# Optimization experiments

Measured on AMD Instinct MI355X. Metric: run time of the kernel, lower is better.

The kernel has to match this reference:

```python
import jax, jax.numpy as jnp
import numpy as np

B, N, FH, H, FO = 8, 1024, 128, 8, 64
FIN = 2 * FH  # f_hid * 2
NEG = -1e9
SLOPE = 0.2  # leaky_relu negative slope (GAT default)


def setup_inputs() -> dict:
    key = jax.random.key(0)
    ks = jax.random.split(key, 10)
    x = jax.random.normal(ks[0], (B, FIN), jnp.float32)
    A = jax.random.randint(ks[1], (B, N, N), 0, 2, jnp.int32)  # 0/1 dense adjacency
    mask_zero = jnp.ones((B, N, 1), jnp.float32)  # node validity mask
    p_atten = jax.random.uniform(ks[2], (B, N), jnp.float32)  # unused in forward body
    e_atten = jax.random.uniform(ks[3], (B, N, FIN), jnp.float32)
    Npost = jax.random.normal(ks[4], (N, FIN), jnp.float32) * np.float32(1.0 / np.sqrt(FIN))  # kaiming-ish
    w = jax.random.normal(ks[5], (H, FIN, FO), jnp.float32) * np.float32(1.0 / np.sqrt(FIN))
    a_src = jax.random.normal(ks[6], (H, FO), jnp.float32) * np.float32(0.1)
    a_dst = jax.random.normal(ks[7], (H, FO), jnp.float32) * np.float32(0.1)
    bias = jnp.zeros((FO,), jnp.float32)
    return {"x": x, "A": A, "mask_zero": mask_zero, "p_atten": p_atten,
            "e_atten": e_atten, "Npost": Npost, "w": w, "a_src": a_src,
            "a_dst": a_dst, "bias": bias}


def reference(x, A, mask_zero, p_atten, e_atten, Npost, w, a_src, a_dst, bias):
    # broadcast-mul feature gating: x [B,FIN] repeated over N posts, gated by Npost*e_atten
    recx = x[:, None, :] * (Npost[None, :, :] * e_atten)          # [B,N,FIN]
    # BatchGAT (DeepInf-style multi-head graph attention, dropout disabled / eval mode)
    h = jnp.einsum('bnf,hfo->bhno', recx, w)                      # [B,H,N,FO]
    s = jnp.einsum('bhno,ho->bhn', h, a_src)                      # src attention term
    d = jnp.einsum('bhno,ho->bhn', h, a_dst)                      # dst attention term
    logits = jax.nn.leaky_relu(s[:, :, :, None] + d[:, :, None, :], SLOPE)  # [B,H,N,N]
    adj = (A > 0)[:, None, :, :]                                  # [B,1,N,N]
    logits = jnp.where(adj, logits, NEG)
    attn = jax.nn.softmax(logits, axis=-1)                        # masked row softmax
    out = jnp.einsum('bhnm,bhmo->bhno', attn, h) + bias           # aggregate neighbors
    out = out.mean(axis=1)                                        # average heads -> [B,N,FO]
    return out * mask_zero                                        # zero padded nodes
```

## Files before the change

kernel.cpp:

```cpp
#include <hip/hip_runtime.h>

typedef __attribute__((ext_vector_type(8))) short          bf16x8;
typedef __attribute__((ext_vector_type(8))) unsigned short u16x8;
typedef __attribute__((ext_vector_type(4))) unsigned short u16x4;
typedef __attribute__((ext_vector_type(4))) float          f32x4;
typedef __attribute__((ext_vector_type(4))) unsigned int   u32x4;

union U8 { u16x8 u; bf16x8 b; u32x4 w; };
union U4 { u16x4 u; unsigned w[2]; };

__device__ __forceinline__ unsigned short f2bf(float f){
  unsigned u = __float_as_uint(f);
  return (unsigned short)((u + 0x7fffu + ((u >> 16) & 1u)) >> 16);
}
__device__ __forceinline__ unsigned pack_bf16(float lo, float hi){
  unsigned a = __float_as_uint(hi) + 0x8000u;
  unsigned b = __float_as_uint(lo) + 0x8000u;
  return __builtin_amdgcn_perm(a, b, 0x07060302u);
}
__device__ __forceinline__ unsigned maskpack(float e0, float e1, unsigned m){
  unsigned r;
  asm("v_cvt_pk_bf16_f32 %0, %1, %2" : "=v"(r) : "v"(e0), "v"(e1));
  return r & m;
}

#define NN  1024
#define FIN 256
#define NH  8
#define FO  64

__global__ __launch_bounds__(256) void stage0(
    const float* __restrict__ w, const int* __restrict__ A,
    unsigned short* __restrict__ wfrag, unsigned long long* __restrict__ Abits)
{
  const int tid = blockIdx.x * 256 + threadIdx.x;
  if (tid < 16384){
    const int lane = tid & 63, ss = (tid >> 6) & 3, kc = (tid >> 8) & 7, h = tid >> 11;
    const int o = 16 * ss + (lane & 15);
    const int f = kc * 32 + (lane >> 4) * 8;
    u16x8 r;
    #pragma unroll
    for (int j = 0; j < 8; j++) r[j] = f2bf(w[(h * FIN + f + j) * FO + o]);
    *(u16x8*)(wfrag + tid * 8) = r;
  }
  for (int i = tid; i < 8388608; i += 262144){
    unsigned long long m = __ballot(A[i] > 0);
    if ((threadIdx.x & 63) == 0) Abits[i >> 6] = m;
  }
}

__global__ __launch_bounds__(512, 4) void stageA(
    const float* __restrict__ x, const float* __restrict__ e_at,
    const float* __restrict__ Np, const unsigned short* __restrict__ wfrag,
    const float* __restrict__ a_src, const float* __restrict__ a_dst,
    unsigned short* __restrict__ hT,
    float* __restrict__ Rt, float* __restrict__ expd, float* __restrict__ expd2)
{
  __shared__ unsigned short rex[16 * 264];
  const int t = threadIdx.x;
  const int n0 = blockIdx.x * 16, b = blockIdx.y;

  {
    const int row = t >> 5, f0 = (t & 31) * 8;
    const int nrow = n0 + row;
    const float* ep = e_at + (b * NN + nrow) * FIN + f0;
    const float* qp = Np + nrow * FIN + f0;
    const float* xp = x + b * FIN + f0;
    f32x4 e0 = *(const f32x4*)ep, e1 = *(const f32x4*)(ep + 4);
    f32x4 q0 = *(const f32x4*)qp, q1 = *(const f32x4*)(qp + 4);
    f32x4 x0 = *(const f32x4*)xp, x1 = *(const f32x4*)(xp + 4);
    u16x8 r;
    #pragma unroll
    for (int j = 0; j < 4; j++){
      r[j]     = f2bf(e0[j] * q0[j] * x0[j]);
      r[j + 4] = f2bf(e1[j] * q1[j] * x1[j]);
    }
    *(u16x8*)(rex + row * 264 + f0) = r;
  }
  __syncthreads();

  const int h = t >> 6, lane = t & 63, quad = lane >> 4, l15 = lane & 15;
  const unsigned short* wf = wfrag + h * 16384 + lane * 8;

  f32x4 acc[4] = {};
  #pragma unroll
  for (int kc = 0; kc < 8; kc++){
    U8 a0, bf[4];
    a0.u = *(const u16x8*)(rex + l15 * 264 + kc * 32 + quad * 8);
    #pragma unroll
    for (int ss = 0; ss < 4; ss++) bf[ss].u = *(const u16x8*)(wf + (kc * 4 + ss) * 512);
    #pragma unroll
    for (int ss = 0; ss < 4; ss++)
      acc[ss] = __builtin_amdgcn_mfma_f32_16x16x32_bf16(a0.b, bf[ss].b, acc[ss], 0, 0, 0);
  }

  {
    const int mtile = blockIdx.x >> 1, moff = (blockIdx.x & 1) * 16;
    unsigned short* pan = hT + (size_t)(((b * NH + h) * 32 + mtile) * 64) * 32;
    #pragma unroll
    for (int ss = 0; ss < 4; ss++){
      U4 v;
      v.w[0] = pack_bf16(acc[ss][0], acc[ss][1]);
      v.w[1] = pack_bf16(acc[ss][2], acc[ss][3]);
      *(u16x4*)(pan + (16 * ss + l15) * 32 + moff + quad * 4) = v.u;
    }
  }

  float as4[4], ad4[4];
  #pragma unroll
  for (int ss = 0; ss < 4; ss++){
    as4[ss] = a_src[h * FO + 16 * ss + l15];
    ad4[ss] = a_dst[h * FO + 16 * ss + l15];
  }
  #pragma unroll
  for (int i = 0; i < 4; i++){
    float ps = 0.f, pd = 0.f;
    #pragma unroll
    for (int ss = 0; ss < 4; ss++){ ps += acc[ss][i] * as4[ss]; pd += acc[ss][i] * ad4[ss]; }
    #pragma unroll
    for (int off = 1; off < 16; off <<= 1){
      ps += __shfl_xor(ps, off);
      pd += __shfl_xor(pd, off);
    }
    if (l15 == 0){
      const int idx = (b * NH + h) * NN + n0 + quad * 4 + i;
      Rt[idx]    = __expf(0.8f * ps);
      expd[idx]  = __expf(pd);
      expd2[idx] = __expf(0.2f * pd);
    }
  }
}

__global__ __launch_bounds__(256, 4) void stageB(
    const unsigned* __restrict__ Aw,
    const unsigned short* __restrict__ hT,
    const float* __restrict__ Rt,
    const float* __restrict__ expd, const float* __restrict__ expd2,
    float* __restrict__ hpart)
{
  __shared__ float smem[4288];
  __shared__ __align__(8) unsigned lut[16][2];

  const int fid = blockIdx.x;
  const int b = fid & 7, h = (fid >> 3) & 7, rt = fid >> 6;
  const int n0 = rt * 64;

  const int t = threadIdx.x;
  const int w = t >> 6, lane = t & 63, quad = lane >> 4, l15 = lane & 15;
  const int rw = w & 1, mh = w >> 1;
  const int nb = n0 + rw * 32;

  if (t < 16){
    lut[t][0] = (t & 1 ? 0xFFFFu : 0u) | (t & 2 ? 0xFFFF0000u : 0u);
    lut[t][1] = (t & 4 ? 0xFFFFu : 0u) | (t & 8 ? 0xFFFF0000u : 0u);
  }
  {
    const float* s1 = expd  + (b * NH + h) * NN;
    const float* s2 = expd2 + (b * NH + h) * NN;
    *(f32x4*)(smem + t * 4)        = *(const f32x4*)(s1 + t * 4);
    *(f32x4*)(smem + 1024 + t * 4) = *(const f32x4*)(s2 + t * 4);
  }
  __syncthreads();

  const int hb = (b * NH + h) * NN;
  const float Rv0 = Rt[hb + nb + l15];
  const float Rv1 = Rt[hb + nb + 16 + l15];
  const unsigned short* pb = hT + (size_t)(b * NH + h) * 65536 + l15 * 32 + quad * 8;
  const float* edh = smem + quad * 8;
  const float* e2h = smem + 1024 + quad * 8;
  const unsigned* awp = Aw + (b * NN + nb) * 32;
  const int c0 = mh * 16;
  const int qs = quad * 8;

  U8 pan[4];
  #pragma unroll
  for (int ss = 0; ss < 4; ss++)
    pan[ss].u = *(const u16x8*)(pb + (size_t)c0 * 2048 + ss * 512);
  unsigned mw0 = awp[l15 * 32 + c0];
  unsigned mw1 = awp[(16 + l15) * 32 + c0];

  U8 ones;
  #pragma unroll
  for (int j = 0; j < 8; j++) ones.u[j] = 0x3F80;

  f32x4 acc0[4] = {}, acc1[4] = {};
  f32x4 accl0 = {}, accl1 = {};

  for (int cc = 0; cc < 16; cc++){
    const int c = c0 + cc;
    const unsigned am0 = (mw0 >> qs) & 0xFF;
    const unsigned am1 = (mw1 >> qs) & 0xFF;
    const uint2 la0 = *(const uint2*)&lut[am0 & 15][0];
    const uint2 lb0 = *(const uint2*)&lut[(am0 >> 4) & 15][0];
    const uint2 la1 = *(const uint2*)&lut[am1 & 15][0];
    const uint2 lb1 = *(const uint2*)&lut[(am1 >> 4) & 15][0];
    if (cc + 1 < 16){
      mw0 = awp[l15 * 32 + c + 1];
      mw1 = awp[(16 + l15) * 32 + c + 1];
    }
    const f32x4 d01 = *(const f32x4*)(edh + c * 32);
    const f32x4 d23 = *(const f32x4*)(edh + c * 32 + 4);
    const f32x4 g01 = *(const f32x4*)(e2h + c * 32);
    const f32x4 g23 = *(const f32x4*)(e2h + c * 32 + 4);
    {
      const f32x4 p01 = Rv0 * d01, p23 = Rv0 * d23;
      U8 p;
      p.w[0] = maskpack(fmaxf(p01[0], g01[0]), fmaxf(p01[1], g01[1]), la0.x);
      p.w[1] = maskpack(fmaxf(p01[2], g01[2]), fmaxf(p01[3], g01[3]), la0.y);
      p.w[2] = maskpack(fmaxf(p23[0], g23[0]), fmaxf(p23[1], g23[1]), lb0.x);
      p.w[3] = maskpack(fmaxf(p23[2], g23[2]), fmaxf(p23[3], g23[3]), lb0.y);
      #pragma unroll
      for (int ss = 0; ss < 4; ss++)
        acc0[ss] = __builtin_amdgcn_mfma_f32_16x16x32_bf16(p.b, pan[ss].b, acc0[ss], 0, 0, 0);
      accl0 = __builtin_amdgcn_mfma_f32_16x16x32_bf16(p.b, ones.b, accl0, 0, 0, 0);
    }
    {
      const f32x4 p01 = Rv1 * d01, p23 = Rv1 * d23;
      U8 p;
      p.w[0] = maskpack(fmaxf(p01[0], g01[0]), fmaxf(p01[1], g01[1]), la1.x);
      p.w[1] = maskpack(fmaxf(p01[2], g01[2]), fmaxf(p01[3], g01[3]), la1.y);
      p.w[2] = maskpack(fmaxf(p23[0], g23[0]), fmaxf(p23[1], g23[1]), lb1.x);
      p.w[3] = maskpack(fmaxf(p23[2], g23[2]), fmaxf(p23[3], g23[3]), lb1.y);
      #pragma unroll
      for (int ss = 0; ss < 4; ss++)
        acc1[ss] = __builtin_amdgcn_mfma_f32_16x16x32_bf16(p.b, pan[ss].b, acc1[ss], 0, 0, 0);
      accl1 = __builtin_amdgcn_mfma_f32_16x16x32_bf16(p.b, ones.b, accl1, 0, 0, 0);
    }
    if (cc + 1 < 16){
      #pragma unroll
      for (int ss = 0; ss < 4; ss++)
        pan[ss].u = *(const u16x8*)(pb + (size_t)(c + 1) * 2048 + ss * 512);
    }
  }

  __syncthreads();

  float* den = smem + 4160;
  if (l15 == 0){
    #pragma unroll
    for (int i = 0; i < 4; i++){
      den[mh * 64 + rw * 32 + quad * 4 + i]      = accl0[i];
      den[mh * 64 + rw * 32 + 16 + quad * 4 + i] = accl1[i];
    }
  }
  if (mh == 1){
    #pragma unroll
    for (int i = 0; i < 4; i++){
      const int r0 = rw * 32 + quad * 4 + i;
      #pragma unroll
      for (int ss = 0; ss < 4; ss++){
        smem[r0 * 65 + ss * 16 + l15]        = acc0[ss][i];
        smem[(r0 + 16) * 65 + ss * 16 + l15] = acc1[ss][i];
      }
    }
  }
  __syncthreads();

  if (mh == 0){
    float* hp = hpart + ((size_t)(b * NH + h) * NN + nb) * FO;
    #pragma unroll
    for (int i = 0; i < 4; i++){
      const int r = quad * 4 + i;
      const float ia = 1.0f / (den[rw * 32 + r] + den[64 + rw * 32 + r]);
      const float ib = 1.0f / (den[rw * 32 + 16 + r] + den[64 + rw * 32 + 16 + r]);
      #pragma unroll
      for (int ss = 0; ss < 4; ss++){
        hp[(size_t)r * FO + ss * 16 + l15] =
            (acc0[ss][i] + smem[(rw * 32 + r) * 65 + ss * 16 + l15]) * ia;
        hp[(size_t)(16 + r) * FO + ss * 16 + l15] =
            (acc1[ss][i] + smem[(rw * 32 + 16 + r) * 65 + ss * 16 + l15]) * ib;
      }
    }
  }
}

__global__ __launch_bounds__(256) void stageC(
    const float* __restrict__ hpart, const float* __restrict__ bias,
    const float* __restrict__ mz, float* __restrict__ out)
{
  const int tid = blockIdx.x * 256 + threadIdx.x;
  const int o4 = (tid & 15) * 4;
  const int n  = (tid >> 4) & 1023;
  const int b  = tid >> 14;
  const size_t nf = (size_t)n * FO + o4;
  f32x4 s = {};
  #pragma unroll
  for (int h = 0; h < NH; h++)
    s += *(const f32x4*)(hpart + (size_t)(b * NH + h) * NN * FO + nf);
  const f32x4 bv = *(const f32x4*)(bias + o4);
  const float m = mz[b * NN + n];
  f32x4 r;
  #pragma unroll
  for (int j = 0; j < 4; j++) r[j] = (0.125f * s[j] + bv[j]) * m;
  *(f32x4*)(out + (size_t)b * NN * FO + nf) = r;
}

extern "C" void kernel_launch(void* const* d_in, const int* in_sizes, int n_in,
                              void* d_out, int out_size, void* d_ws, size_t ws_size,
                              hipStream_t stream)
{
  (void)in_sizes; (void)n_in; (void)out_size; (void)ws_size;
  const float* x    = (const float*)d_in[0];
  const int*   A    = (const int*)d_in[1];
  const float* mz   = (const float*)d_in[2];
  const float* e_at = (const float*)d_in[4];
  const float* Np   = (const float*)d_in[5];
  const float* w    = (const float*)d_in[6];
  const float* asrc = (const float*)d_in[7];
  const float* adst = (const float*)d_in[8];
  const float* bias = (const float*)d_in[9];
  float* out = (float*)d_out;

  char* ws = (char*)d_ws;
  unsigned short* wfrag = (unsigned short*)ws;
  unsigned short* hT    = (unsigned short*)(ws + 262144);
  float* Rt    = (float*)(ws + 8650752);
  float* expd  = (float*)(ws + 8912896);
  float* expd2 = (float*)(ws + 9175040);
  unsigned long long* Abits = (unsigned long long*)(ws + 9437184);
  float* hpart = (float*)(ws + 10485760);

  stage0<<<dim3(1024), dim3(256), 0, stream>>>(w, A, wfrag, Abits);
  stageA<<<dim3(64, 8), dim3(512), 0, stream>>>(x, e_at, Np, wfrag, asrc, adst,
                                                hT, Rt, expd, expd2);
  stageB<<<dim3(1024), dim3(256), 0, stream>>>((const unsigned*)Abits, hT,
                                               Rt, expd, expd2, hpart);
  stageC<<<dim3(512), dim3(256), 0, stream>>>(hpart, bias, mz, out);
}
```

Baseline: 153.0 us.

## Move adjacency bit-packing into stageA and double-buffer stageB panel loads

```diff
diff --git a/kernel.cpp b/kernel.cpp
--- a/kernel.cpp
+++ b/kernel.cpp
@@ -30,29 +30,23 @@
 #define FO  64
 
 __global__ __launch_bounds__(256) void stage0(
-    const float* __restrict__ w, const int* __restrict__ A,
-    unsigned short* __restrict__ wfrag, unsigned long long* __restrict__ Abits)
+    const float* __restrict__ w, unsigned short* __restrict__ wfrag)
 {
   const int tid = blockIdx.x * 256 + threadIdx.x;
-  if (tid < 16384){
-    const int lane = tid & 63, ss = (tid >> 6) & 3, kc = (tid >> 8) & 7, h = tid >> 11;
-    const int o = 16 * ss + (lane & 15);
-    const int f = kc * 32 + (lane >> 4) * 8;
-    u16x8 r;
-    #pragma unroll
-    for (int j = 0; j < 8; j++) r[j] = f2bf(w[(h * FIN + f + j) * FO + o]);
-    *(u16x8*)(wfrag + tid * 8) = r;
-  }
-  for (int i = tid; i < 8388608; i += 262144){
-    unsigned long long m = __ballot(A[i] > 0);
-    if ((threadIdx.x & 63) == 0) Abits[i >> 6] = m;
-  }
+  const int lane = tid & 63, ss = (tid >> 6) & 3, kc = (tid >> 8) & 7, h = tid >> 11;
+  const int o = 16 * ss + (lane & 15);
+  const int f = kc * 32 + (lane >> 4) * 8;
+  u16x8 r;
+  #pragma unroll
+  for (int j = 0; j < 8; j++) r[j] = f2bf(w[(h * FIN + f + j) * FO + o]);
+  *(u16x8*)(wfrag + tid * 8) = r;
 }
 
 __global__ __launch_bounds__(512, 4) void stageA(
     const float* __restrict__ x, const float* __restrict__ e_at,
     const float* __restrict__ Np, const unsigned short* __restrict__ wfrag,
     const float* __restrict__ a_src, const float* __restrict__ a_dst,
+    const int* __restrict__ A, unsigned long long* __restrict__ Abits,
     unsigned short* __restrict__ hT,
     float* __restrict__ Rt, float* __restrict__ expd, float* __restrict__ expd2)
 {
@@ -129,6 +123,16 @@
       expd2[idx] = __expf(0.2f * pd);
     }
   }
+
+  {
+    const int seg = (b * 64 + blockIdx.x) * 16384;
+    #pragma unroll 4
+    for (int k = 0; k < 32; k++){
+      const int i = seg + k * 512 + t;
+      unsigned long long m = __ballot(A[i] > 0);
+      if ((t & 63) == 0) Abits[i >> 6] = m;
+    }
+  }
 }
 
 __global__ __launch_bounds__(256, 4) void stageB(
@@ -172,12 +176,13 @@
   const int c0 = mh * 16;
   const int qs = quad * 8;
 
-  U8 pan[4];
+  U8 panc[4], pann[4];
   #pragma unroll
   for (int ss = 0; ss < 4; ss++)
-    pan[ss].u = *(const u16x8*)(pb + (size_t)c0 * 2048 + ss * 512);
-  unsigned mw0 = awp[l15 * 32 + c0];
-  unsigned mw1 = awp[(16 + l15) * 32 + c0];
+    panc[ss].u = *(const u16x8*)(pb + (size_t)c0 * 2048 + ss * 512);
+  unsigned mwc0 = awp[l15 * 32 + c0];
+  unsigned mwc1 = awp[(16 + l15) * 32 + c0];
+  unsigned mwn0, mwn1;
 
   U8 ones;
   #pragma unroll
@@ -186,18 +191,22 @@
   f32x4 acc0[4] = {}, acc1[4] = {};
   f32x4 accl0 = {}, accl1 = {};
 
+  #pragma unroll
   for (int cc = 0; cc < 16; cc++){
     const int c = c0 + cc;
-    const unsigned am0 = (mw0 >> qs) & 0xFF;
-    const unsigned am1 = (mw1 >> qs) & 0xFF;
+    if (cc + 1 < 16){
+      #pragma unroll
+      for (int ss = 0; ss < 4; ss++)
+        pann[ss].u = *(const u16x8*)(pb + (size_t)(c + 1) * 2048 + ss * 512);
+      mwn0 = awp[l15 * 32 + c + 1];
+      mwn1 = awp[(16 + l15) * 32 + c + 1];
+    }
+    const unsigned am0 = (mwc0 >> qs) & 0xFF;
+    const unsigned am1 = (mwc1 >> qs) & 0xFF;
     const uint2 la0 = *(const uint2*)&lut[am0 & 15][0];
     const uint2 lb0 = *(const uint2*)&lut[(am0 >> 4) & 15][0];
     const uint2 la1 = *(const uint2*)&lut[am1 & 15][0];
     const uint2 lb1 = *(const uint2*)&lut[(am1 >> 4) & 15][0];
-    if (cc + 1 < 16){
-      mw0 = awp[l15 * 32 + c + 1];
-      mw1 = awp[(16 + l15) * 32 + c + 1];
-    }
     const f32x4 d01 = *(const f32x4*)(edh + c * 32);
     const f32x4 d23 = *(const f32x4*)(edh + c * 32 + 4);
     const f32x4 g01 = *(const f32x4*)(e2h + c * 32);
@@ -211,7 +220,7 @@
       p.w[3] = maskpack(fmaxf(p23[2], g23[2]), fmaxf(p23[3], g23[3]), lb0.y);
       #pragma unroll
       for (int ss = 0; ss < 4; ss++)
-        acc0[ss] = __builtin_amdgcn_mfma_f32_16x16x32_bf16(p.b, pan[ss].b, acc0[ss], 0, 0, 0);
+        acc0[ss] = __builtin_amdgcn_mfma_f32_16x16x32_bf16(p.b, panc[ss].b, acc0[ss], 0, 0, 0);
       accl0 = __builtin_amdgcn_mfma_f32_16x16x32_bf16(p.b, ones.b, accl0, 0, 0, 0);
     }
     {
@@ -223,13 +232,13 @@
       p.w[3] = maskpack(fmaxf(p23[2], g23[2]), fmaxf(p23[3], g23[3]), lb1.y);
       #pragma unroll
       for (int ss = 0; ss < 4; ss++)
-        acc1[ss] = __builtin_amdgcn_mfma_f32_16x16x32_bf16(p.b, pan[ss].b, acc1[ss], 0, 0, 0);
+        acc1[ss] = __builtin_amdgcn_mfma_f32_16x16x32_bf16(p.b, panc[ss].b, acc1[ss], 0, 0, 0);
       accl1 = __builtin_amdgcn_mfma_f32_16x16x32_bf16(p.b, ones.b, accl1, 0, 0, 0);
     }
     if (cc + 1 < 16){
       #pragma unroll
-      for (int ss = 0; ss < 4; ss++)
-        pan[ss].u = *(const u16x8*)(pb + (size_t)(c + 1) * 2048 + ss * 512);
+      for (int ss = 0; ss < 4; ss++) panc[ss] = pann[ss];
+      mwc0 = mwn0; mwc1 = mwn1;
     }
   }
 
@@ -320,9 +329,9 @@
   unsigned long long* Abits = (unsigned long long*)(ws + 9437184);
   float* hpart = (float*)(ws + 10485760);
 
-  stage0<<<dim3(1024), dim3(256), 0, stream>>>(w, A, wfrag, Abits);
+  stage0<<<dim3(64), dim3(256), 0, stream>>>(w, wfrag);
   stageA<<<dim3(64, 8), dim3(512), 0, stream>>>(x, e_at, Np, wfrag, asrc, adst,
-                                                hT, Rt, expd, expd2);
+                                                A, Abits, hT, Rt, expd, expd2);
   stageB<<<dim3(1024), dim3(256), 0, stream>>>((const unsigned*)Abits, hT,
                                                Rt, expd, expd2, hpart);
   stageC<<<dim3(512), dim3(256), 0, stream>>>(hpart, bias, mz, out);
```

After: 151.3 us. Within noise of the previous version (-1.1%).

## Fuse head-mean into attention kernel via last-block counter and reshape grids

Applied to the files above, without the earlier changes.

```diff
diff --git a/kernel.cpp b/kernel.cpp
--- a/kernel.cpp
+++ b/kernel.cpp
@@ -29,11 +29,14 @@
 #define NH  8
 #define FO  64
 
-__global__ __launch_bounds__(256) void stage0(
+__global__ __launch_bounds__(256) void prep(
     const float* __restrict__ w, const int* __restrict__ A,
-    unsigned short* __restrict__ wfrag, unsigned long long* __restrict__ Abits)
+    unsigned short* __restrict__ wfrag, unsigned long long* __restrict__ Abits,
+    int* __restrict__ cnt)
 {
-  const int tid = blockIdx.x * 256 + threadIdx.x;
+  const int bid = blockIdx.x, t = threadIdx.x;
+  const int tid = bid * 256 + t;
+  if (tid < 128) cnt[tid] = 0;
   if (tid < 16384){
     const int lane = tid & 63, ss = (tid >> 6) & 3, kc = (tid >> 8) & 7, h = tid >> 11;
     const int o = 16 * ss + (lane & 15);
@@ -43,13 +46,16 @@
     for (int j = 0; j < 8; j++) r[j] = f2bf(w[(h * FIN + f + j) * FO + o]);
     *(u16x8*)(wfrag + tid * 8) = r;
   }
-  for (int i = tid; i < 8388608; i += 262144){
+  const int base = (bid & 7) * 1048576 + (bid >> 3) * 8192;
+  #pragma unroll 4
+  for (int k = 0; k < 32; k++){
+    const int i = base + k * 256 + t;
     unsigned long long m = __ballot(A[i] > 0);
-    if ((threadIdx.x & 63) == 0) Abits[i >> 6] = m;
-  }
-}
-
-__global__ __launch_bounds__(512, 4) void stageA(
+    if ((t & 63) == 0) Abits[i >> 6] = m;
+  }
+}
+
+__global__ __launch_bounds__(256, 4) void gemmA(
     const float* __restrict__ x, const float* __restrict__ e_at,
     const float* __restrict__ Np, const unsigned short* __restrict__ wfrag,
     const float* __restrict__ a_src, const float* __restrict__ a_dst,
@@ -58,28 +64,33 @@
 {
   __shared__ unsigned short rex[16 * 264];
   const int t = threadIdx.x;
-  const int n0 = blockIdx.x * 16, b = blockIdx.y;
+  const int fid = blockIdx.x;
+  const int b = fid & 7, tile = (fid >> 3) & 63, hg = fid >> 9;
+  const int n0 = tile * 16;
 
   {
-    const int row = t >> 5, f0 = (t & 31) * 8;
-    const int nrow = n0 + row;
-    const float* ep = e_at + (b * NN + nrow) * FIN + f0;
-    const float* qp = Np + nrow * FIN + f0;
-    const float* xp = x + b * FIN + f0;
-    f32x4 e0 = *(const f32x4*)ep, e1 = *(const f32x4*)(ep + 4);
-    f32x4 q0 = *(const f32x4*)qp, q1 = *(const f32x4*)(qp + 4);
-    f32x4 x0 = *(const f32x4*)xp, x1 = *(const f32x4*)(xp + 4);
-    u16x8 r;
-    #pragma unroll
-    for (int j = 0; j < 4; j++){
-      r[j]     = f2bf(e0[j] * q0[j] * x0[j]);
-      r[j + 4] = f2bf(e1[j] * q1[j] * x1[j]);
-    }
-    *(u16x8*)(rex + row * 264 + f0) = r;
-  }
-  __syncthreads();
-
-  const int h = t >> 6, lane = t & 63, quad = lane >> 4, l15 = lane & 15;
+    #pragma unroll
+    for (int rep = 0; rep < 2; rep++){
+      const int row = rep * 8 + (t >> 5), f0 = (t & 31) * 8;
+      const int nrow = n0 + row;
+      const float* ep = e_at + (b * NN + nrow) * FIN + f0;
+      const float* qp = Np + nrow * FIN + f0;
+      const float* xp = x + b * FIN + f0;
+      f32x4 e0 = *(const f32x4*)ep, e1 = *(const f32x4*)(ep + 4);
+      f32x4 q0 = *(const f32x4*)qp, q1 = *(const f32x4*)(qp + 4);
+      f32x4 x0 = *(const f32x4*)xp, x1 = *(const f32x4*)(xp + 4);
+      u16x8 r;
+      #pragma unroll
+      for (int j = 0; j < 4; j++){
+        r[j]     = f2bf(e0[j] * q0[j] * x0[j]);
+        r[j + 4] = f2bf(e1[j] * q1[j] * x1[j]);
+      }
+      *(u16x8*)(rex + row * 264 + f0) = r;
+    }
+  }
+  __syncthreads();
+
+  const int h = hg * 4 + (t >> 6), lane = t & 63, quad = lane >> 4, l15 = lane & 15;
   const unsigned short* wf = wfrag + h * 16384 + lane * 8;
 
   f32x4 acc[4] = {};
@@ -95,7 +106,7 @@
   }
 
   {
-    const int mtile = blockIdx.x >> 1, moff = (blockIdx.x & 1) * 16;
+    const int mtile = tile >> 1, moff = (tile & 1) * 16;
     unsigned short* pan = hT + (size_t)(((b * NH + h) * 32 + mtile) * 64) * 32;
     #pragma unroll
     for (int ss = 0; ss < 4; ss++){
@@ -131,15 +142,18 @@
   }
 }
 
-__global__ __launch_bounds__(256, 4) void stageB(
+__global__ __launch_bounds__(256, 4) void attnB(
     const unsigned* __restrict__ Aw,
     const unsigned short* __restrict__ hT,
     const float* __restrict__ Rt,
     const float* __restrict__ expd, const float* __restrict__ expd2,
-    float* __restrict__ hpart)
+    float* __restrict__ hpart, int* __restrict__ cnt,
+    const float* __restrict__ bias, const float* __restrict__ mz,
+    float* __restrict__ out)
 {
   __shared__ float smem[4288];
   __shared__ __align__(8) unsigned lut[16][2];
+  __shared__ int tick;
 
   const int fid = blockIdx.x;
   const int b = fid & 7, h = (fid >> 3) & 7, rt = fid >> 6;
@@ -186,6 +200,7 @@
   f32x4 acc0[4] = {}, acc1[4] = {};
   f32x4 accl0 = {}, accl1 = {};
 
+  #pragma unroll
   for (int cc = 0; cc < 16; cc++){
     const int c = c0 + cc;
     const unsigned am0 = (mw0 >> qs) & 0xFF;
@@ -272,27 +287,30 @@
       }
     }
   }
-}
-
-__global__ __launch_bounds__(256) void stageC(
-    const float* __restrict__ hpart, const float* __restrict__ bias,
-    const float* __restrict__ mz, float* __restrict__ out)
-{
-  const int tid = blockIdx.x * 256 + threadIdx.x;
-  const int o4 = (tid & 15) * 4;
-  const int n  = (tid >> 4) & 1023;
-  const int b  = tid >> 14;
-  const size_t nf = (size_t)n * FO + o4;
-  f32x4 s = {};
-  #pragma unroll
-  for (int h = 0; h < NH; h++)
-    s += *(const f32x4*)(hpart + (size_t)(b * NH + h) * NN * FO + nf);
-  const f32x4 bv = *(const f32x4*)(bias + o4);
-  const float m = mz[b * NN + n];
-  f32x4 r;
-  #pragma unroll
-  for (int j = 0; j < 4; j++) r[j] = (0.125f * s[j] + bv[j]) * m;
-  *(f32x4*)(out + (size_t)b * NN * FO + nf) = r;
+
+  __threadfence();
+  __syncthreads();
+  if (t == 0) tick = atomicAdd(&cnt[b * 16 + rt], 1);
+  __syncthreads();
+  if (tick == 7){
+    __threadfence();
+    #pragma unroll
+    for (int k = 0; k < 4; k++){
+      const int idx = k * 256 + t;
+      const int row = idx >> 4, o4 = (idx & 15) * 4;
+      const float* hp0 = hpart + ((size_t)(b * NH) * NN + n0 + row) * FO + o4;
+      f32x4 s = {};
+      #pragma unroll
+      for (int hh = 0; hh < NH; hh++)
+        s += *(const f32x4*)(hp0 + (size_t)hh * NN * FO);
+      const f32x4 bv = *(const f32x4*)(bias + o4);
+      const float m = mz[b * NN + n0 + row];
+      f32x4 r;
+      #pragma unroll
+      for (int j = 0; j < 4; j++) r[j] = (0.125f * s[j] + bv[j]) * m;
+      *(f32x4*)(out + (size_t)(b * NN + n0 + row) * FO + o4) = r;
+    }
+  }
 }
 
 extern "C" void kernel_launch(void* const* d_in, const int* in_sizes, int n_in,
@@ -319,11 +337,12 @@
   float* expd2 = (float*)(ws + 9175040);
   unsigned long long* Abits = (unsigned long long*)(ws + 9437184);
   float* hpart = (float*)(ws + 10485760);
-
-  stage0<<<dim3(1024), dim3(256), 0, stream>>>(w, A, wfrag, Abits);
-  stageA<<<dim3(64, 8), dim3(512), 0, stream>>>(x, e_at, Np, wfrag, asrc, adst,
-                                                hT, Rt, expd, expd2);
-  stageB<<<dim3(1024), dim3(256), 0, stream>>>((const unsigned*)Abits, hT,
-                                               Rt, expd, expd2, hpart);
-  stageC<<<dim3(512), dim3(256), 0, stream>>>(hpart, bias, mz, out);
-}
+  int*   cnt   = (int*)(ws + 27262976);
+
+  prep <<<dim3(1024), dim3(256), 0, stream>>>(w, A, wfrag, Abits, cnt);
+  gemmA<<<dim3(1024), dim3(256), 0, stream>>>(x, e_at, Np, wfrag, asrc, adst,
+                                              hT, Rt, expd, expd2);
+  attnB<<<dim3(1024), dim3(256), 0, stream>>>((const unsigned*)Abits, hT,
+                                              Rt, expd, expd2, hpart, cnt,
+                                              bias, mz, out);
+}
```

Result: slower. 278.1 us (+81.8%).

## Split projection GEMM across head groups and make adjacency packing block-contiguous

Applied to the files above, without the earlier changes.

```diff
diff --git a/kernel.cpp b/kernel.cpp
--- a/kernel.cpp
+++ b/kernel.cpp
@@ -29,11 +29,12 @@
 #define NH  8
 #define FO  64
 
-__global__ __launch_bounds__(256) void stage0(
+__global__ __launch_bounds__(256) void prep(
     const float* __restrict__ w, const int* __restrict__ A,
     unsigned short* __restrict__ wfrag, unsigned long long* __restrict__ Abits)
 {
-  const int tid = blockIdx.x * 256 + threadIdx.x;
+  const int bid = blockIdx.x, t = threadIdx.x;
+  const int tid = bid * 256 + t;
   if (tid < 16384){
     const int lane = tid & 63, ss = (tid >> 6) & 3, kc = (tid >> 8) & 7, h = tid >> 11;
     const int o = 16 * ss + (lane & 15);
@@ -43,13 +44,16 @@
     for (int j = 0; j < 8; j++) r[j] = f2bf(w[(h * FIN + f + j) * FO + o]);
     *(u16x8*)(wfrag + tid * 8) = r;
   }
-  for (int i = tid; i < 8388608; i += 262144){
+  const int base = (bid & 7) * 1048576 + (bid >> 3) * 8192;
+  #pragma unroll 4
+  for (int k = 0; k < 32; k++){
+    const int i = base + k * 256 + t;
     unsigned long long m = __ballot(A[i] > 0);
-    if ((threadIdx.x & 63) == 0) Abits[i >> 6] = m;
-  }
-}
-
-__global__ __launch_bounds__(512, 4) void stageA(
+    if ((t & 63) == 0) Abits[i >> 6] = m;
+  }
+}
+
+__global__ __launch_bounds__(256, 4) void gemmA(
     const float* __restrict__ x, const float* __restrict__ e_at,
     const float* __restrict__ Np, const unsigned short* __restrict__ wfrag,
     const float* __restrict__ a_src, const float* __restrict__ a_dst,
@@ -58,28 +62,33 @@
 {
   __shared__ unsigned short rex[16 * 264];
   const int t = threadIdx.x;
-  const int n0 = blockIdx.x * 16, b = blockIdx.y;
+  const int fid = blockIdx.x;
+  const int b = fid & 7, tile = (fid >> 3) & 63, hg = fid >> 9;
+  const int n0 = tile * 16;
 
   {
-    const int row = t >> 5, f0 = (t & 31) * 8;
-    const int nrow = n0 + row;
-    const float* ep = e_at + (b * NN + nrow) * FIN + f0;
-    const float* qp = Np + nrow * FIN + f0;
-    const float* xp = x + b * FIN + f0;
-    f32x4 e0 = *(const f32x4*)ep, e1 = *(const f32x4*)(ep + 4);
-    f32x4 q0 = *(const f32x4*)qp, q1 = *(const f32x4*)(qp + 4);
-    f32x4 x0 = *(const f32x4*)xp, x1 = *(const f32x4*)(xp + 4);
-    u16x8 r;
-    #pragma unroll
-    for (int j = 0; j < 4; j++){
-      r[j]     = f2bf(e0[j] * q0[j] * x0[j]);
-      r[j + 4] = f2bf(e1[j] * q1[j] * x1[j]);
-    }
-    *(u16x8*)(rex + row * 264 + f0) = r;
+    #pragma unroll
+    for (int rep = 0; rep < 2; rep++){
+      const int row = rep * 8 + (t >> 5), f0 = (t & 31) * 8;
+      const int nrow = n0 + row;
+      const float* ep = e_at + (b * NN + nrow) * FIN + f0;
+      const float* qp = Np + nrow * FIN + f0;
+      const float* xp = x + b * FIN + f0;
+      f32x4 e0 = *(const f32x4*)ep, e1 = *(const f32x4*)(ep + 4);
+      f32x4 q0 = *(const f32x4*)qp, q1 = *(const f32x4*)(qp + 4);
+      f32x4 x0 = *(const f32x4*)xp, x1 = *(const f32x4*)(xp + 4);
+      u16x8 r;
+      #pragma unroll
+      for (int j = 0; j < 4; j++){
+        r[j]     = f2bf(e0[j] * q0[j] * x0[j]);
+        r[j + 4] = f2bf(e1[j] * q1[j] * x1[j]);
+      }
+      *(u16x8*)(rex + row * 264 + f0) = r;
+    }
   }
   __syncthreads();
 
-  const int h = t >> 6, lane = t & 63, quad = lane >> 4, l15 = lane & 15;
+  const int h = hg * 4 + (t >> 6), lane = t & 63, quad = lane >> 4, l15 = lane & 15;
   const unsigned short* wf = wfrag + h * 16384 + lane * 8;
 
   f32x4 acc[4] = {};
@@ -95,7 +104,7 @@
   }
 
   {
-    const int mtile = blockIdx.x >> 1, moff = (blockIdx.x & 1) * 16;
+    const int mtile = tile >> 1, moff = (tile & 1) * 16;
     unsigned short* pan = hT + (size_t)(((b * NH + h) * 32 + mtile) * 64) * 32;
     #pragma unroll
     for (int ss = 0; ss < 4; ss++){
@@ -131,7 +140,7 @@
   }
 }
 
-__global__ __launch_bounds__(256, 4) void stageB(
+__global__ __launch_bounds__(256, 4) void attnB(
     const unsigned* __restrict__ Aw,
     const unsigned short* __restrict__ hT,
     const float* __restrict__ Rt,
@@ -186,6 +195,7 @@
   f32x4 acc0[4] = {}, acc1[4] = {};
   f32x4 accl0 = {}, accl1 = {};
 
+  #pragma unroll
   for (int cc = 0; cc < 16; cc++){
     const int c = c0 + cc;
     const unsigned am0 = (mw0 >> qs) & 0xFF;
@@ -320,10 +330,10 @@
   unsigned long long* Abits = (unsigned long long*)(ws + 9437184);
   float* hpart = (float*)(ws + 10485760);
 
-  stage0<<<dim3(1024), dim3(256), 0, stream>>>(w, A, wfrag, Abits);
-  stageA<<<dim3(64, 8), dim3(512), 0, stream>>>(x, e_at, Np, wfrag, asrc, adst,
-                                                hT, Rt, expd, expd2);
-  stageB<<<dim3(1024), dim3(256), 0, stream>>>((const unsigned*)Abits, hT,
-                                               Rt, expd, expd2, hpart);
+  prep <<<dim3(1024), dim3(256), 0, stream>>>(w, A, wfrag, Abits);
+  gemmA<<<dim3(1024), dim3(256), 0, stream>>>(x, e_at, Np, wfrag, asrc, adst,
+                                              hT, Rt, expd, expd2);
+  attnB<<<dim3(1024), dim3(256), 0, stream>>>((const unsigned*)Abits, hT,
+                                              Rt, expd, expd2, hpart);
   stageC<<<dim3(512), dim3(256), 0, stream>>>(hpart, bias, mz, out);
 }
```

Result: no change. 154.3 us (+0.9%).
